# Optimization experiments

Measured on AMD Instinct MI355X. Metric: run time of the kernel, lower is better.

Reference implementation:

```python
import jax, jax.numpy as jnp
import numpy as np

B, D, C = 1024, 512, 512


def _per_sample_ce(xi, yi, W, b):
    # categorical cross-entropy of a single sample through a linear+softmax head
    logits = xi @ W + b                      # [C]
    return -jnp.sum(yi * jax.nn.log_softmax(logits))


def setup_inputs() -> dict:
    key = jax.random.key(0)
    k1, k2, k3 = jax.random.split(key, 3)
    x = jax.random.normal(k1, (B, D), dtype=jnp.float32)
    labels = jax.random.randint(k2, (B,), 0, C)
    y_true = jax.nn.one_hot(labels, C, dtype=jnp.float32)  # [B, C]
    W = jax.random.normal(k3, (D, C), dtype=jnp.float32) * 0.02
    b = jnp.zeros((C,), dtype=jnp.float32)
    return {"x": x, "y_true": y_true, "W": W, "b": b}


def reference(x, y_true, W, b):
    # Per-sample gradient norm of the loss w.r.t. parameter_list = [W, b].
    # Equivalent to the Keras slow path (map_fn over samples of K.gradients),
    # vectorized with vmap over the batch dimension.
    def gnorm(xi, yi):
        gW, gb = jax.grad(lambda p: _per_sample_ce(xi, yi, p[0], p[1]))((W, b))
        return jnp.sqrt(jnp.sum(gW * gW) + jnp.sum(gb * gb))

    grads = jax.vmap(gnorm)(x, y_true)       # [B]
    return grads[:, None]                    # [B, 1] as in compute_output_shape
```

## Files before the change

### kernel.cpp

```cpp
#include <hip/hip_runtime.h>

#define Bn 1024
#define Dn 512
#define Cn 512
#define Sn 8
#define NT 512
#define NBLK (Bn / Sn)

__device__ __forceinline__ float waveSum(float v) {
    #pragma unroll
    for (int off = 32; off > 0; off >>= 1) v += __shfl_xor(v, off, 64);
    return v;
}
__device__ __forceinline__ float waveMax(float v) {
    #pragma unroll
    for (int off = 32; off > 0; off >>= 1) v = fmaxf(v, __shfl_xor(v, off, 64));
    return v;
}

__global__ __launch_bounds__(NT) void gnorm_one(
    const float* __restrict__ x,
    const float* __restrict__ y,
    const float* __restrict__ W,
    const float* __restrict__ bias,
    float* __restrict__ out)
{
    __shared__ float xt[Dn][16];
    __shared__ float red[Sn][8];
    __shared__ float xn2s[Sn];

    const int tid = threadIdx.x;
    const int wv  = tid >> 6;
    const int l   = tid & 63;
    const int s0  = blockIdx.x * Sn;

    {
        const int s  = tid & 7;
        const int k0 = (tid >> 3) * 8;
        const float* xp = &x[(size_t)(s0 + s) * Dn + k0];
        float4 a = *(const float4*)xp;
        float4 b = *(const float4*)(xp + 4);
        xt[k0 + 0][s] = a.x; xt[k0 + 1][s] = a.y; xt[k0 + 2][s] = a.z; xt[k0 + 3][s] = a.w;
        xt[k0 + 4][s] = b.x; xt[k0 + 5][s] = b.y; xt[k0 + 6][s] = b.z; xt[k0 + 7][s] = b.w;
    }
    {
        const float* xr = &x[(size_t)(s0 + wv) * Dn + l * 8];
        float4 a = *(const float4*)xr;
        float4 b = *(const float4*)(xr + 4);
        float ss = a.x*a.x + a.y*a.y + a.z*a.z + a.w*a.w
                 + b.x*b.x + b.y*b.y + b.z*b.z + b.w*b.w;
        ss = waveSum(ss);
        if (l == 0) xn2s[wv] = ss;
    }
    __syncthreads();

    const int c = tid;
    const float* wp = &W[c];
    float acc[8] = {0.f, 0.f, 0.f, 0.f, 0.f, 0.f, 0.f, 0.f};

    for (int k = 0; k < Dn; k += 16) {
        float wr[16];
        #pragma unroll
        for (int i = 0; i < 16; ++i) wr[i] = wp[(size_t)(k + i) * Cn];
        #pragma unroll
        for (int i = 0; i < 16; ++i) {
            float4 xa = *(const float4*)&xt[k + i][0];
            float4 xb = *(const float4*)&xt[k + i][4];
            acc[0] = fmaf(xa.x, wr[i], acc[0]);
            acc[1] = fmaf(xa.y, wr[i], acc[1]);
            acc[2] = fmaf(xa.z, wr[i], acc[2]);
            acc[3] = fmaf(xa.w, wr[i], acc[3]);
            acc[4] = fmaf(xb.x, wr[i], acc[4]);
            acc[5] = fmaf(xb.y, wr[i], acc[5]);
            acc[6] = fmaf(xb.z, wr[i], acc[6]);
            acc[7] = fmaf(xb.w, wr[i], acc[7]);
        }
    }

    const float bc = bias[c];
    float z[8];
    #pragma unroll
    for (int s = 0; s < 8; ++s) z[s] = acc[s] + bc;

    #pragma unroll
    for (int s = 0; s < 8; ++s) {
        float m = waveMax(z[s]);
        if (l == 0) red[s][wv] = m;
    }
    __syncthreads();
    float mx[8];
    #pragma unroll
    for (int s = 0; s < 8; ++s) {
        float m = red[s][0];
        #pragma unroll
        for (int w = 1; w < 8; ++w) m = fmaxf(m, red[s][w]);
        mx[s] = m;
    }
    __syncthreads();

    float e[8];
    #pragma unroll
    for (int s = 0; s < 8; ++s) {
        e[s] = __expf(z[s] - mx[s]);
        float sv = waveSum(e[s]);
        if (l == 0) red[s][wv] = sv;
    }
    __syncthreads();
    float inv[8];
    #pragma unroll
    for (int s = 0; s < 8; ++s) {
        float dv = red[s][0];
        #pragma unroll
        for (int w = 1; w < 8; ++w) dv += red[s][w];
        inv[s] = 1.0f / dv;
    }
    __syncthreads();

    #pragma unroll
    for (int s = 0; s < 8; ++s) {
        float g = e[s] * inv[s] - y[(size_t)(s0 + s) * Cn + c];
        float gs = waveSum(g * g);
        if (l == 0) red[s][wv] = gs;
    }
    __syncthreads();

    if (tid < Sn) {
        float gsq = red[tid][0];
        #pragma unroll
        for (int w = 1; w < 8; ++w) gsq += red[tid][w];
        out[s0 + tid] = sqrtf((xn2s[tid] + 1.0f) * gsq);
    }
}

extern "C" void kernel_launch(void* const* d_in, const int* in_sizes, int n_in,
                              void* d_out, int out_size, void* d_ws, size_t ws_size,
                              hipStream_t stream) {
    const float* x  = (const float*)d_in[0];
    const float* y  = (const float*)d_in[1];
    const float* W  = (const float*)d_in[2];
    const float* b  = (const float*)d_in[3];
    float* out = (float*)d_out;
    gnorm_one<<<dim3(NBLK), dim3(NT), 0, stream>>>(x, y, W, b, out);
}
```

Baseline: 90.40 us.

## Halve samples per block and read x directly instead of staging in LDS

Reduces samples per block from 8 to 4, doubling the grid to 256 blocks so more CUs are busy on the 1024-row batch. Drops the shared-memory transpose of x and instead reads x rows straight from global memory (wave-uniform addresses, likely scalar loads) inside the GEMV loop. It also removes the initial barrier. In exchange, W is re-read from memory twice as many times overall, and each W column load is reused across only 4 samples instead of 8.

Result: faster. 84.63 us (-6.4%).

```diff
diff --git a/kernel.cpp b/kernel.cpp
--- a/kernel.cpp
+++ b/kernel.cpp
@@ -3,7 +3,7 @@
 #define Bn 1024
 #define Dn 512
 #define Cn 512
-#define Sn 8
+#define Sn 4
 #define NT 512
 #define NBLK (Bn / Sn)
 
@@ -25,7 +25,6 @@
     const float* __restrict__ bias,
     float* __restrict__ out)
 {
-    __shared__ float xt[Dn][16];
     __shared__ float red[Sn][8];
     __shared__ float xn2s[Sn];
 
@@ -34,16 +33,7 @@
     const int l   = tid & 63;
     const int s0  = blockIdx.x * Sn;
 
-    {
-        const int s  = tid & 7;
-        const int k0 = (tid >> 3) * 8;
-        const float* xp = &x[(size_t)(s0 + s) * Dn + k0];
-        float4 a = *(const float4*)xp;
-        float4 b = *(const float4*)(xp + 4);
-        xt[k0 + 0][s] = a.x; xt[k0 + 1][s] = a.y; xt[k0 + 2][s] = a.z; xt[k0 + 3][s] = a.w;
-        xt[k0 + 4][s] = b.x; xt[k0 + 5][s] = b.y; xt[k0 + 6][s] = b.z; xt[k0 + 7][s] = b.w;
-    }
-    {
+    if (wv < Sn) {
         const float* xr = &x[(size_t)(s0 + wv) * Dn + l * 8];
         float4 a = *(const float4*)xr;
         float4 b = *(const float4*)(xr + 4);
@@ -52,11 +42,11 @@
         ss = waveSum(ss);
         if (l == 0) xn2s[wv] = ss;
     }
-    __syncthreads();
 
     const int c = tid;
-    const float* wp = &W[c];
-    float acc[8] = {0.f, 0.f, 0.f, 0.f, 0.f, 0.f, 0.f, 0.f};
+    const float* wp  = &W[c];
+    const float* xr0 = &x[(size_t)s0 * Dn];
+    float acc[4] = {0.f, 0.f, 0.f, 0.f};
 
     for (int k = 0; k < Dn; k += 16) {
         float wr[16];
@@ -64,33 +54,27 @@
         for (int i = 0; i < 16; ++i) wr[i] = wp[(size_t)(k + i) * Cn];
         #pragma unroll
         for (int i = 0; i < 16; ++i) {
-            float4 xa = *(const float4*)&xt[k + i][0];
-            float4 xb = *(const float4*)&xt[k + i][4];
-            acc[0] = fmaf(xa.x, wr[i], acc[0]);
-            acc[1] = fmaf(xa.y, wr[i], acc[1]);
-            acc[2] = fmaf(xa.z, wr[i], acc[2]);
-            acc[3] = fmaf(xa.w, wr[i], acc[3]);
-            acc[4] = fmaf(xb.x, wr[i], acc[4]);
-            acc[5] = fmaf(xb.y, wr[i], acc[5]);
-            acc[6] = fmaf(xb.z, wr[i], acc[6]);
-            acc[7] = fmaf(xb.w, wr[i], acc[7]);
+            #pragma unroll
+            for (int s = 0; s < Sn; ++s)
+                acc[s] = fmaf(xr0[(size_t)s * Dn + k + i], wr[i], acc[s]);
         }
     }
 
     const float bc = bias[c];
-    float z[8];
+    float z[Sn];
     #pragma unroll
-    for (int s = 0; s < 8; ++s) z[s] = acc[s] + bc;
+    for (int s = 0; s < Sn; ++s) z[s] = acc[s] + bc;
 
+    __syncthreads();
     #pragma unroll
-    for (int s = 0; s < 8; ++s) {
+    for (int s = 0; s < Sn; ++s) {
         float m = waveMax(z[s]);
         if (l == 0) red[s][wv] = m;
     }
     __syncthreads();
-    float mx[8];
+    float mx[Sn];
     #pragma unroll
-    for (int s = 0; s < 8; ++s) {
+    for (int s = 0; s < Sn; ++s) {
         float m = red[s][0];
         #pragma unroll
         for (int w = 1; w < 8; ++w) m = fmaxf(m, red[s][w]);
@@ -98,17 +82,17 @@
     }
     __syncthreads();
 
-    float e[8];
+    float e[Sn];
     #pragma unroll
-    for (int s = 0; s < 8; ++s) {
+    for (int s = 0; s < Sn; ++s) {
         e[s] = __expf(z[s] - mx[s]);
         float sv = waveSum(e[s]);
         if (l == 0) red[s][wv] = sv;
     }
     __syncthreads();
-    float inv[8];
+    float inv[Sn];
     #pragma unroll
-    for (int s = 0; s < 8; ++s) {
+    for (int s = 0; s < Sn; ++s) {
         float dv = red[s][0];
         #pragma unroll
         for (int w = 1; w < 8; ++w) dv += red[s][w];
@@ -117,7 +101,7 @@
     __syncthreads();
 
     #pragma unroll
-    for (int s = 0; s < 8; ++s) {
+    for (int s = 0; s < Sn; ++s) {
         float g = e[s] * inv[s] - y[(size_t)(s0 + s) * Cn + c];
         float gs = waveSum(g * g);
         if (l == 0) red[s][wv] = gs;
```
